# Performance work log

Measured on AMD Instinct MI355X. Metric: run time of the kernel, lower is better.

Reference implementation:

```python
import jax, jax.numpy as jnp
import numpy as np

B, S = 1024, 512
V, E, H, T = 50000, 300, 800, 50


def setup_inputs() -> dict:
    key = jax.random.key(0)
    ks = jax.random.split(key, 8)
    ids = jax.random.randint(ks[0], (B, S), 0, V, dtype=jnp.int64 if jax.config.jax_enable_x64 else jnp.int32)
    return {
        "ids": ids,
        "rho": jax.random.normal(ks[1], (V, E), jnp.float32) * 0.02,
        "alpha": jax.random.normal(ks[2], (T, E), jnp.float32) * 0.02,
        "W1": jax.random.normal(ks[3], (E, H), jnp.float32) * 0.05,
        "b1": jnp.zeros((H,), jnp.float32),
        "Wmu": jax.random.normal(ks[4], (H, T), jnp.float32) * 0.05,
        "bmu": jnp.zeros((T,), jnp.float32),
        "Wlv": jax.random.normal(ks[5], (H, T), jnp.float32) * 0.05,
        "blv": jnp.zeros((T,), jnp.float32),
    }


def reference(ids, rho, alpha, W1, b1, Wmu, bmu, Wlv, blv):
    b, s = ids.shape
    v = rho.shape[0]
    # bag-of-words histogram: scatter-add instead of dense one_hot+reduce_sum
    bows = jnp.zeros((b, v), rho.dtype).at[jnp.arange(b)[:, None], ids].add(1.0)
    # zero out special tokens 1 and 2 (original: x * (1 - sum(one_hot([1,2]))))
    bows = bows.at[:, jnp.array([1, 2])].set(0.0)
    normal_bows = bows / jnp.sum(bows, axis=-1, keepdims=True)
    # encoder (eval mode: dropout is identity)
    x = jnp.einsum('bv,ve->be', normal_bows, rho)
    h = jax.nn.relu(x @ W1 + b1)
    mu_theta = h @ Wmu + bmu
    logsigma_theta = h @ Wlv + blv
    kl_theta = -0.5 * jnp.sum(1.0 + logsigma_theta - mu_theta**2 - jnp.exp(logsigma_theta), axis=-1)
    # reparameterize (eval/inference mode): z = mu
    theta = jax.nn.softmax(mu_theta, axis=-1)  # [B, T]
    beta = jax.nn.softmax(jnp.einsum('te,ve->tv', alpha, rho), axis=-1)  # [T, V]
    lookup = jnp.log(theta @ beta + 1e-5)  # [B, V]
    recon_loss = -jnp.sum(lookup * bows, axis=-1)
    loss = jnp.mean(recon_loss) + jnp.mean(kl_theta)
    return theta, loss
```

## Files before the change

kernel.cpp:

```cpp
#include <hip/hip_runtime.h>
#include <math.h>


#define Bn 1024
#define Sn 512
#define Vn 50000
#define En 300
#define Hn 800
#define Tn 50
#define KP 320
#define BSTR 64
#define W1FRAG_N (50 * 10 * 64 * 8)
#define WFRAG_N  (8 * 25 * 64 * 8)
#define NRANGE 8
#define CASTB 7813
#define K4B 3128

typedef __bf16 bf16x8 __attribute__((ext_vector_type(8)));
typedef float  f32x4  __attribute__((ext_vector_type(4)));
typedef float  f32x2  __attribute__((ext_vector_type(2)));

__device__ __forceinline__ float waveReduceSum(float v) {
    #pragma unroll
    for (int off = 32; off > 0; off >>= 1) v += __shfl_xor(v, off, 64);
    return v;
}
__device__ __forceinline__ float waveReduceMax(float v) {
    #pragma unroll
    for (int off = 32; off > 0; off >>= 1) v = fmaxf(v, __shfl_xor(v, off, 64));
    return v;
}
__device__ __forceinline__ unsigned short f2bf(float x) {
    unsigned u = __float_as_uint(x);
    return (unsigned short)((u + 0x7FFFu + ((u >> 16) & 1u)) >> 16);
}
__device__ __forceinline__ float bf_lo(unsigned u) { return __uint_as_float(u << 16); }
__device__ __forceinline__ float bf_hi(unsigned u) { return __uint_as_float(u & 0xFFFF0000u); }
__device__ __forceinline__ int lane_prefix(unsigned long long m) {
    return __builtin_amdgcn_mbcnt_hi((unsigned)(m >> 32),
           __builtin_amdgcn_mbcnt_lo((unsigned)m, 0));
}

#define PKACC(u) { \
    c0 += (f32x2){bf_lo((u).x), bf_hi((u).x)}; \
    c1 += (f32x2){bf_lo((u).y), bf_hi((u).y)}; \
    c2 += (f32x2){bf_lo((u).z), bf_hi((u).z)}; \
    c3 += (f32x2){bf_lo((u).w), bf_hi((u).w)}; }

__global__ __launch_bounds__(256) void ka_init(
        const float4* __restrict__ rho4, unsigned short* __restrict__ rhoh,
        const float* __restrict__ alpha, const float* __restrict__ W1,
        const float* __restrict__ Wmu, const float* __restrict__ Wlv,
        unsigned short* __restrict__ bfrag, unsigned short* __restrict__ w1frag,
        unsigned short* __restrict__ wfrag, float* __restrict__ topicsumR,
        float* __restrict__ loss) {
    if (blockIdx.x < CASTB) {
        const int i = blockIdx.x * 256 + threadIdx.x;
        if (i < Vn * (KP / 8)) {
            int v = i / (KP / 8), s8 = i - v * (KP / 8);
            int c = s8 * 8;
            ushort4 o0 = {0, 0, 0, 0}, o1 = {0, 0, 0, 0};
            if (c < En) {
                float4 r = rho4[v * (En / 4) + s8 * 2];
                o0.x = f2bf(r.x); o0.y = f2bf(r.y); o0.z = f2bf(r.z); o0.w = f2bf(r.w);
            }
            if (c + 4 < En) {
                float4 r = rho4[v * (En / 4) + s8 * 2 + 1];
                o1.x = f2bf(r.x); o1.y = f2bf(r.y); o1.z = f2bf(r.z); o1.w = f2bf(r.w);
            }
            uint4 st;
            st.x = (unsigned)o0.x | ((unsigned)o0.y << 16);
            st.y = (unsigned)o0.z | ((unsigned)o0.w << 16);
            st.z = (unsigned)o1.x | ((unsigned)o1.y << 16);
            st.w = (unsigned)o1.z | ((unsigned)o1.w << 16);
            *(uint4*)(rhoh + (size_t)v * KP + c) = st;
        }
        return;
    }
    const int gid = (blockIdx.x - CASTB) * 256 + threadIdx.x;
    if (gid < 512) topicsumR[gid] = 0.f;
    if (gid == 520) *loss = 0.f;
    if (gid < 4 * 10 * 64 * 8) {
        int j = gid & 7;
        int lane = (gid >> 3) & 63;
        int rest = gid >> 9;
        int kt = rest % 10, w = rest / 10;
        int t = 16 * w + (lane & 15);
        int e = kt * 32 + (lane >> 4) * 8 + j;
        bfrag[gid] = (t < Tn && e < En) ? f2bf(alpha[t * En + e]) : (unsigned short)0;
    }
    if (gid < W1FRAG_N) {
        int j = gid & 7, lane = (gid >> 3) & 63, rest = gid >> 9;
        int kt = rest % 10, nt = rest / 10;
        int e = kt * 32 + (lane >> 4) * 8 + j;
        int hcol = nt * 16 + (lane & 15);
        w1frag[gid] = (e < En) ? f2bf(W1[e * Hn + hcol]) : (unsigned short)0;
    } else {
        int g2 = gid - W1FRAG_N;
        if (g2 < WFRAG_N) {
            int j = g2 & 7, lane = (g2 >> 3) & 63, rest = g2 >> 9;
            int kt = rest % 25, nt = rest / 25;
            int k = kt * 32 + (lane >> 4) * 8 + j;
            int t = (nt & 3) * 16 + (lane & 15);
            float val = 0.f;
            if (t < Tn) val = (nt < 4) ? Wmu[k * Tn + t] : Wlv[k * Tn + t];
            wfrag[g2] = f2bf(val);
        }
    }
}

__global__ __launch_bounds__(256) void kb_beta_tokens(
        const unsigned short* __restrict__ rhoh,
        const unsigned short* __restrict__ bfrag,
        unsigned int* __restrict__ betaU32, float* __restrict__ topicsumR,
        const int* __restrict__ ids, int* __restrict__ toks,
        int* __restrict__ cnt, float* __restrict__ xbarP) {
    __shared__ unsigned short trans[16 * 66];
    __shared__ __align__(16) int sid[Sn];
    __shared__ int sfid[Sn];
    __shared__ __align__(16) float xred[4][320];
    __shared__ int scount, sfull;
    const int tid = threadIdx.x;
    const int wave = tid >> 6, lane = tid & 63;

    if (blockIdx.x < K4B) {
        const int x = blockIdx.x & 7;
        const int n = blockIdx.x >> 3;
        const int tile = ((x * 3125) >> 3) + n;
        if (tile >= (((x + 1) * 3125) >> 3)) return;
        const int quad = lane >> 4, l15 = lane & 15;
        const int v0 = tile * 16;
        const unsigned short* arow = rhoh + (size_t)(v0 + l15) * KP + quad * 8;
        f32x4 acc = {0.f, 0.f, 0.f, 0.f};
        #pragma unroll
        for (int kt = 0; kt < 10; ++kt) {
            bf16x8 a = *(const bf16x8*)(arow + kt * 32);
            bf16x8 bv = *(const bf16x8*)(bfrag + ((wave * 10 + kt) * 64 + lane) * 8);
            acc = __builtin_amdgcn_mfma_f32_16x16x32_bf16(a, bv, acc, 0, 0, 0);
        }
        float ts = 0.f;
        #pragma unroll
        for (int r = 0; r < 4; ++r) {
            float ev = expf(acc[r]);
            ts += ev;
            trans[(quad * 4 + r) * 66 + 16 * wave + l15] = f2bf(ev);
        }
        ts += __shfl_xor(ts, 16, 64);
        ts += __shfl_xor(ts, 32, 64);
        const int t = 16 * wave + l15;
        if (lane < 16 && t < Tn)
            atomicAdd(&topicsumR[x * 64 + t], ts);
        __syncthreads();
        unsigned int* dst = betaU32 + (size_t)v0 * 32;
        const unsigned int* tr32 = (const unsigned int*)trans;
        for (int i = tid; i < 16 * 32; i += 256)
            __builtin_nontemporal_store(tr32[(i >> 5) * 33 + (i & 31)], &dst[i]);
        return;
    }
    const int blk = blockIdx.x - K4B;
    const int r = blk & (NRANGE - 1), b = blk >> 3;
    const int lo = ((r * 3125) >> 3) * 16;
    const int hi = (((r + 1) * 3125) >> 3) * 16;
    if (tid == 0) { scount = 0; sfull = 0; }
    __syncthreads();
    #pragma unroll
    for (int s0 = 0; s0 < Sn; s0 += 256) {
        int id = __builtin_nontemporal_load(&ids[b * Sn + s0 + tid]);
        bool val = (id != 1 && id != 2);
        bool inr = val && id >= lo && id < hi;
        unsigned long long mb = __ballot(inr);
        int pre = lane_prefix(mb);
        int wc = __popcll(mb);
        int base = 0;
        if (lane == 0 && wc) base = atomicAdd(&scount, wc);
        base = __shfl(base, 0, 64);
        if (inr) sid[base + pre] = id;
        if (r == 0) {
            unsigned long long fb = __ballot(val);
            int fpre = lane_prefix(fb);
            int fwc = __popcll(fb);
            int fbase = 0;
            if (lane == 0 && fwc) fbase = atomicAdd(&sfull, fwc);
            fbase = __shfl(fbase, 0, 64);
            if (val) sfid[fbase + fpre] = id;
        }
    }
    __syncthreads();
    if (r == 0) {
        const int nf = sfull;
        for (int i = tid; i < nf; i += 256)
            __builtin_nontemporal_store(sfid[i], &toks[b * Sn + i]);
        if (tid == 0) cnt[b] = nf;
    }
    const int m = scount;
    f32x2 c0 = {0.f, 0.f}, c1 = {0.f, 0.f}, c2 = {0.f, 0.f}, c3 = {0.f, 0.f};
    if (lane < 40) {
        const uint4* rb = (const uint4*)rhoh;
        int s = wave;
        for (; s + 12 < m; s += 16) {
            int i0 = sid[s], i1 = sid[s + 4], i2 = sid[s + 8], i3 = sid[s + 12];
            uint4 u0 = rb[(size_t)i0 * 40 + lane];
            uint4 u1 = rb[(size_t)i1 * 40 + lane];
            uint4 u2 = rb[(size_t)i2 * 40 + lane];
            uint4 u3 = rb[(size_t)i3 * 40 + lane];
            PKACC(u0); PKACC(u1); PKACC(u2); PKACC(u3);
        }
        for (; s < m; s += 4) {
            uint4 u = rb[(size_t)sid[s] * 40 + lane];
            PKACC(u);
        }
        float* xw = &xred[wave][lane * 8];
        *(float4*)(xw)     = (float4){c0[0], c0[1], c1[0], c1[1]};
        *(float4*)(xw + 4) = (float4){c2[0], c2[1], c3[0], c3[1]};
    }
    __syncthreads();
    float* xbp = xbarP + ((size_t)b * NRANGE + r) * KP;
    for (int c = tid; c < KP; c += 256)
        __builtin_nontemporal_store(
            xred[0][c] + xred[1][c] + xred[2][c] + xred[3][c], &xbp[c]);
}

__global__ __launch_bounds__(256) void ktail(
        const float* __restrict__ xbarP, const int* __restrict__ cnt,
        const unsigned short* __restrict__ w1frag, const float* __restrict__ b1,
        const unsigned short* __restrict__ wfrag,
        const float* __restrict__ bmu, const float* __restrict__ blv,
        float* __restrict__ theta, float* __restrict__ loss) {
    __shared__ unsigned short xs[16 * 328];
    __shared__ unsigned short hs[16 * 808];
    __shared__ float mlds[16 * 65];
    __shared__ float llds[16 * 65];
    __shared__ float invn[16];
    const int tid = threadIdx.x;
    const int wave = tid >> 6, lane = tid & 63;
    const int quad = lane >> 4, l15 = lane & 15;
    const int b0 = blockIdx.x * 16;
    if (tid < 16) invn[tid] = 1.0f / (float)cnt[b0 + tid];
    __syncthreads();
    for (int i = tid; i < 16 * (KP / 4); i += 256) {
        int row = i / (KP / 4), e4 = (i - row * (KP / 4)) * 4;
        const float* bp = xbarP + ((size_t)(b0 + row) * NRANGE) * KP + e4;
        float sx = 0.f, sy = 0.f, sz = 0.f, sw_ = 0.f;
        #pragma unroll
        for (int rr = 0; rr < NRANGE; ++rr) {
            float4 v = *(const float4*)(bp + rr * KP);
            sx += v.x; sy += v.y; sz += v.z; sw_ += v.w;
        }
        float in = invn[row];
        ushort4 o;
        o.x = f2bf(sx * in); o.y = f2bf(sy * in);
        o.z = f2bf(sz * in); o.w = f2bf(sw_ * in);
        *(ushort4*)&xs[row * 328 + e4] = o;
    }
    __syncthreads();
    {
        const unsigned short* arow = xs + l15 * 328 + quad * 8;
        for (int nt = wave; nt < 50; nt += 4) {
            f32x4 acc = {0.f, 0.f, 0.f, 0.f};
            #pragma unroll
            for (int kt = 0; kt < 10; ++kt) {
                bf16x8 a = *(const bf16x8*)(arow + kt * 32);
                bf16x8 bv = *(const bf16x8*)(w1frag + ((size_t)(nt * 10 + kt) * 64 + lane) * 8);
                acc = __builtin_amdgcn_mfma_f32_16x16x32_bf16(a, bv, acc, 0, 0, 0);
            }
            const int col = nt * 16 + l15;
            const float bias = b1[col];
            #pragma unroll
            for (int r = 0; r < 4; ++r)
                hs[(quad * 4 + r) * 808 + col] = f2bf(fmaxf(acc[r] + bias, 0.f));
        }
    }
    __syncthreads();
    {
        const unsigned short* arow = hs + l15 * 808 + quad * 8;
        f32x4 am = {0.f, 0.f, 0.f, 0.f}, al = {0.f, 0.f, 0.f, 0.f};
        #pragma unroll
        for (int kt = 0; kt < 25; ++kt) {
            bf16x8 a  = *(const bf16x8*)(arow + kt * 32);
            bf16x8 bm = *(const bf16x8*)(wfrag + ((size_t)(wave * 25 + kt) * 64 + lane) * 8);
            bf16x8 bl = *(const bf16x8*)(wfrag + ((size_t)((4 + wave) * 25 + kt) * 64 + lane) * 8);
            am = __builtin_amdgcn_mfma_f32_16x16x32_bf16(a, bm, am, 0, 0, 0);
            al = __builtin_amdgcn_mfma_f32_16x16x32_bf16(a, bl, al, 0, 0, 0);
        }
        const int t = wave * 16 + l15;
        const float bm_ = (t < Tn) ? bmu[t] : 0.f;
        const float bl_ = (t < Tn) ? blv[t] : 0.f;
        #pragma unroll
        for (int r = 0; r < 4; ++r) {
            int row = quad * 4 + r;
            mlds[row * 65 + t] = am[r] + bm_;
            llds[row * 65 + t] = al[r] + bl_;
        }
    }
    __syncthreads();
    const int tt = (lane < Tn) ? lane : (Tn - 1);
    const bool act = (lane < Tn);
    float klacc = 0.f;
    #pragma unroll
    for (int k = 0; k < 4; ++k) {
        int row = wave * 4 + k;
        float mu = mlds[row * 65 + tt];
        float lv = llds[row * 65 + tt];
        float m = waveReduceMax(act ? mu : -1e30f);
        float ex = act ? expf(mu - m) : 0.f;
        float ssum = waveReduceSum(ex);
        if (act) theta[(b0 + row) * Tn + lane] = ex / ssum;
        klacc += waveReduceSum(act ? (1.f + lv - mu * mu - expf(lv)) : 0.f);
    }
    if (lane == 0) atomicAdd(loss, -0.5f * klacc * (1.0f / (float)Bn));
}

__global__ __launch_bounds__(256) void k6_recon(
        const int* __restrict__ toks, const int* __restrict__ cnt,
        const float* __restrict__ theta, const float* __restrict__ topicsumR,
        const unsigned short* __restrict__ betaUh, float* __restrict__ loss) {
    __shared__ float sw[Tn];
    __shared__ float swred[4];
    const int b = blockIdx.x, tid = threadIdx.x;
    if (tid < Tn) {
        float z = 0.f;
        #pragma unroll
        for (int j = 0; j < 8; ++j) z += topicsumR[j * 64 + tid];
        sw[tid] = theta[b * Tn + tid] / z;
    }
    __syncthreads();
    float wr[Tn];
    #pragma unroll
    for (int t = 0; t < Tn; ++t) wr[t] = sw[t];
    float lsum = 0.f;
    const int n = cnt[b];
    for (int i = tid; i < n; i += 256) {
        int v = toks[b * Sn + i];
        const uint4* q = (const uint4*)(betaUh + (size_t)v * BSTR);
        float dot = 0.f;
        #pragma unroll
        for (int k = 0; k < 6; ++k) {
            uint4 u = q[k];
            int t = 8 * k;
            dot += wr[t]     * bf_lo(u.x) + wr[t + 1] * bf_hi(u.x);
            dot += wr[t + 2] * bf_lo(u.y) + wr[t + 3] * bf_hi(u.y);
            dot += wr[t + 4] * bf_lo(u.z) + wr[t + 5] * bf_hi(u.z);
            dot += wr[t + 6] * bf_lo(u.w) + wr[t + 7] * bf_hi(u.w);
        }
        unsigned d = ((const unsigned*)q)[24];
        dot += wr[48] * bf_lo(d) + wr[49] * bf_hi(d);
        lsum += logf(dot + 1e-5f);
    }
    float s = waveReduceSum(lsum);
    const int wave = tid >> 6, lane = tid & 63;
    if (lane == 0) swred[wave] = s;
    __syncthreads();
    if (tid == 0) {
        float tot = swred[0] + swred[1] + swred[2] + swred[3];
        atomicAdd(loss, -tot * (1.0f / (float)Bn));
    }
}

extern "C" void kernel_launch(void* const* d_in, const int* in_sizes, int n_in,
                              void* d_out, int out_size, void* d_ws, size_t ws_size,
                              hipStream_t stream) {
    const int*   ids   = (const int*)d_in[0];
    const float* rho   = (const float*)d_in[1];
    const float* alpha = (const float*)d_in[2];
    const float* W1    = (const float*)d_in[3];
    const float* b1    = (const float*)d_in[4];
    const float* Wmu   = (const float*)d_in[5];
    const float* bmu   = (const float*)d_in[6];
    const float* Wlv   = (const float*)d_in[7];
    const float* blv   = (const float*)d_in[8];

    float* theta = (float*)d_out;
    float* loss  = theta + Bn * Tn;

    char* w = (char*)d_ws;
    float* topicsumR = (float*)w;               w += 8 * 64 * 4;
    unsigned short* bfrag = (unsigned short*)w; w += 4 * 10 * 64 * 8 * 2;
    unsigned short* w1frag = (unsigned short*)w; w += (size_t)W1FRAG_N * 2;
    unsigned short* wfrag = (unsigned short*)w;  w += (size_t)WFRAG_N * 2;
    int*   cnt      = (int*)w;                  w += Bn * 4;
    int*   toks     = (int*)w;                  w += Bn * Sn * 4;
    float* xbarP    = (float*)w;                w += (size_t)Bn * NRANGE * KP * 4;
    unsigned short* rhoh = (unsigned short*)w;  w += (size_t)Vn * KP * 2;
    unsigned int* betaU32 = (unsigned int*)w;   w += (size_t)Vn * 128;

    const int k0grid = (W1FRAG_N + WFRAG_N + 255) / 256;
    ka_init<<<CASTB + k0grid, 256, 0, stream>>>(
        (const float4*)rho, rhoh, alpha, W1, Wmu, Wlv,
        bfrag, w1frag, wfrag, topicsumR, loss);
    kb_beta_tokens<<<K4B + Bn * NRANGE, 256, 0, stream>>>(
        rhoh, bfrag, betaU32, topicsumR, ids, toks, cnt, xbarP);
    ktail<<<64, 256, 0, stream>>>(xbarP, cnt, w1frag, b1, wfrag, bmu, blv,
                                  theta, loss);
    k6_recon<<<Bn, 256, 0, stream>>>(toks, cnt, theta, topicsumR,
                                     (const unsigned short*)betaU32, loss);
}
```

Before: 211.3 us.

## Fuse rho bf16 cast into beta kernel and split token gather kernel

The fp32-to-bf16 conversion of rho moves out of the init kernel and into the beta kernel. Each tile now loads fp32 rho rows, converts them into shared memory, writes the bf16 copy, and feeds the MFMA directly from LDS. The old combined beta/token kernel is split into two launches, kb4_beta and kb1_gather, and the nontemporal stores become plain stores. This avoids a full separate pass that reread rhoh before the beta GEMM, but it adds a kernel launch and serializes the beta and gather work that previously shared one grid.

```diff
diff --git a/kernel.cpp b/kernel.cpp
--- a/kernel.cpp
+++ b/kernel.cpp
@@ -13,7 +13,6 @@
 #define W1FRAG_N (50 * 10 * 64 * 8)
 #define WFRAG_N  (8 * 25 * 64 * 8)
 #define NRANGE 8
-#define CASTB 7813
 #define K4B 3128
 
 typedef __bf16 bf16x8 __attribute__((ext_vector_type(8)));
@@ -47,37 +46,13 @@
     c2 += (f32x2){bf_lo((u).z), bf_hi((u).z)}; \
     c3 += (f32x2){bf_lo((u).w), bf_hi((u).w)}; }
 
-__global__ __launch_bounds__(256) void ka_init(
-        const float4* __restrict__ rho4, unsigned short* __restrict__ rhoh,
+__global__ __launch_bounds__(256) void ka2_init(
         const float* __restrict__ alpha, const float* __restrict__ W1,
         const float* __restrict__ Wmu, const float* __restrict__ Wlv,
         unsigned short* __restrict__ bfrag, unsigned short* __restrict__ w1frag,
         unsigned short* __restrict__ wfrag, float* __restrict__ topicsumR,
         float* __restrict__ loss) {
-    if (blockIdx.x < CASTB) {
-        const int i = blockIdx.x * 256 + threadIdx.x;
-        if (i < Vn * (KP / 8)) {
-            int v = i / (KP / 8), s8 = i - v * (KP / 8);
-            int c = s8 * 8;
-            ushort4 o0 = {0, 0, 0, 0}, o1 = {0, 0, 0, 0};
-            if (c < En) {
-                float4 r = rho4[v * (En / 4) + s8 * 2];
-                o0.x = f2bf(r.x); o0.y = f2bf(r.y); o0.z = f2bf(r.z); o0.w = f2bf(r.w);
-            }
-            if (c + 4 < En) {
-                float4 r = rho4[v * (En / 4) + s8 * 2 + 1];
-                o1.x = f2bf(r.x); o1.y = f2bf(r.y); o1.z = f2bf(r.z); o1.w = f2bf(r.w);
-            }
-            uint4 st;
-            st.x = (unsigned)o0.x | ((unsigned)o0.y << 16);
-            st.y = (unsigned)o0.z | ((unsigned)o0.w << 16);
-            st.z = (unsigned)o1.x | ((unsigned)o1.y << 16);
-            st.w = (unsigned)o1.z | ((unsigned)o1.w << 16);
-            *(uint4*)(rhoh + (size_t)v * KP + c) = st;
-        }
-        return;
-    }
-    const int gid = (blockIdx.x - CASTB) * 256 + threadIdx.x;
+    const int gid = blockIdx.x * 256 + threadIdx.x;
     if (gid < 512) topicsumR[gid] = 0.f;
     if (gid == 520) *loss = 0.f;
     if (gid < 4 * 10 * 64 * 8) {
@@ -109,56 +84,72 @@
     }
 }
 
-__global__ __launch_bounds__(256) void kb_beta_tokens(
-        const unsigned short* __restrict__ rhoh,
+__global__ __launch_bounds__(256) void kb4_beta(
+        const float* __restrict__ rho, unsigned short* __restrict__ rhoh,
         const unsigned short* __restrict__ bfrag,
-        unsigned int* __restrict__ betaU32, float* __restrict__ topicsumR,
-        const int* __restrict__ ids, int* __restrict__ toks,
-        int* __restrict__ cnt, float* __restrict__ xbarP) {
+        unsigned int* __restrict__ betaU32, float* __restrict__ topicsumR) {
+    __shared__ __align__(16) unsigned short xs[16 * 328];
     __shared__ unsigned short trans[16 * 66];
+    const int x = blockIdx.x & 7;
+    const int n = blockIdx.x >> 3;
+    const int tile = ((x * 3125) >> 3) + n;
+    if (tile >= (((x + 1) * 3125) >> 3)) return;
+    const int tid = threadIdx.x;
+    const int wave = tid >> 6, lane = tid & 63;
+    const int quad = lane >> 4, l15 = lane & 15;
+    const int v0 = tile * 16;
+    for (int i = tid; i < 16 * 80; i += 256) {
+        int row = i / 80, s4 = i - row * 80;
+        ushort4 o = {0, 0, 0, 0};
+        if (s4 < 75) {
+            float4 r = *(const float4*)(rho + (size_t)(v0 + row) * En + s4 * 4);
+            o.x = f2bf(r.x); o.y = f2bf(r.y); o.z = f2bf(r.z); o.w = f2bf(r.w);
+        }
+        *(ushort4*)&xs[row * 328 + s4 * 4] = o;
+    }
+    __syncthreads();
+    for (int i = tid; i < 16 * 40; i += 256) {
+        int row = i / 40, c8 = (i - row * 40) * 8;
+        *(uint4*)(rhoh + (size_t)(v0 + row) * KP + c8) = *(const uint4*)&xs[row * 328 + c8];
+    }
+    const unsigned short* arow = xs + l15 * 328 + quad * 8;
+    f32x4 acc = {0.f, 0.f, 0.f, 0.f};
+    #pragma unroll
+    for (int kt = 0; kt < 10; ++kt) {
+        bf16x8 a = *(const bf16x8*)(arow + kt * 32);
+        bf16x8 bv = *(const bf16x8*)(bfrag + ((wave * 10 + kt) * 64 + lane) * 8);
+        acc = __builtin_amdgcn_mfma_f32_16x16x32_bf16(a, bv, acc, 0, 0, 0);
+    }
+    float ts = 0.f;
+    #pragma unroll
+    for (int r = 0; r < 4; ++r) {
+        float ev = expf(acc[r]);
+        ts += ev;
+        trans[(quad * 4 + r) * 66 + 16 * wave + l15] = f2bf(ev);
+    }
+    ts += __shfl_xor(ts, 16, 64);
+    ts += __shfl_xor(ts, 32, 64);
+    const int t = 16 * wave + l15;
+    if (lane < 16 && t < Tn)
+        atomicAdd(&topicsumR[x * 64 + t], ts);
+    __syncthreads();
+    unsigned int* dst = betaU32 + (size_t)v0 * 32;
+    const unsigned int* tr32 = (const unsigned int*)trans;
+    for (int i = tid; i < 16 * 32; i += 256)
+        dst[i] = tr32[(i >> 5) * 33 + (i & 31)];
+}
+
+__global__ __launch_bounds__(256) void kb1_gather(
+        const unsigned short* __restrict__ rhoh, const int* __restrict__ ids,
+        int* __restrict__ toks, int* __restrict__ cnt,
+        float* __restrict__ xbarP) {
     __shared__ __align__(16) int sid[Sn];
     __shared__ int sfid[Sn];
     __shared__ __align__(16) float xred[4][320];
     __shared__ int scount, sfull;
     const int tid = threadIdx.x;
     const int wave = tid >> 6, lane = tid & 63;
-
-    if (blockIdx.x < K4B) {
-        const int x = blockIdx.x & 7;
-        const int n = blockIdx.x >> 3;
-        const int tile = ((x * 3125) >> 3) + n;
-        if (tile >= (((x + 1) * 3125) >> 3)) return;
-        const int quad = lane >> 4, l15 = lane & 15;
-        const int v0 = tile * 16;
-        const unsigned short* arow = rhoh + (size_t)(v0 + l15) * KP + quad * 8;
-        f32x4 acc = {0.f, 0.f, 0.f, 0.f};
-        #pragma unroll
-        for (int kt = 0; kt < 10; ++kt) {
-            bf16x8 a = *(const bf16x8*)(arow + kt * 32);
-            bf16x8 bv = *(const bf16x8*)(bfrag + ((wave * 10 + kt) * 64 + lane) * 8);
-            acc = __builtin_amdgcn_mfma_f32_16x16x32_bf16(a, bv, acc, 0, 0, 0);
-        }
-        float ts = 0.f;
-        #pragma unroll
-        for (int r = 0; r < 4; ++r) {
-            float ev = expf(acc[r]);
-            ts += ev;
-            trans[(quad * 4 + r) * 66 + 16 * wave + l15] = f2bf(ev);
-        }
-        ts += __shfl_xor(ts, 16, 64);
-        ts += __shfl_xor(ts, 32, 64);
-        const int t = 16 * wave + l15;
-        if (lane < 16 && t < Tn)
-            atomicAdd(&topicsumR[x * 64 + t], ts);
-        __syncthreads();
-        unsigned int* dst = betaU32 + (size_t)v0 * 32;
-        const unsigned int* tr32 = (const unsigned int*)trans;
-        for (int i = tid; i < 16 * 32; i += 256)
-            __builtin_nontemporal_store(tr32[(i >> 5) * 33 + (i & 31)], &dst[i]);
-        return;
-    }
-    const int blk = blockIdx.x - K4B;
-    const int r = blk & (NRANGE - 1), b = blk >> 3;
+    const int r = blockIdx.x & (NRANGE - 1), b = blockIdx.x >> 3;
     const int lo = ((r * 3125) >> 3) * 16;
     const int hi = (((r + 1) * 3125) >> 3) * 16;
     if (tid == 0) { scount = 0; sfull = 0; }
@@ -188,8 +179,7 @@
     __syncthreads();
     if (r == 0) {
         const int nf = sfull;
-        for (int i = tid; i < nf; i += 256)
-            __builtin_nontemporal_store(sfid[i], &toks[b * Sn + i]);
+        for (int i = tid; i < nf; i += 256) toks[b * Sn + i] = sfid[i];
         if (tid == 0) cnt[b] = nf;
     }
     const int m = scount;
@@ -216,8 +206,7 @@
     __syncthreads();
     float* xbp = xbarP + ((size_t)b * NRANGE + r) * KP;
     for (int c = tid; c < KP; c += 256)
-        __builtin_nontemporal_store(
-            xred[0][c] + xred[1][c] + xred[2][c] + xred[3][c], &xbp[c]);
+        xbp[c] = xred[0][c] + xred[1][c] + xred[2][c] + xred[3][c];
 }
 
 __global__ __launch_bounds__(256) void ktail(
@@ -384,11 +373,10 @@
     unsigned int* betaU32 = (unsigned int*)w;   w += (size_t)Vn * 128;
 
     const int k0grid = (W1FRAG_N + WFRAG_N + 255) / 256;
-    ka_init<<<CASTB + k0grid, 256, 0, stream>>>(
-        (const float4*)rho, rhoh, alpha, W1, Wmu, Wlv,
-        bfrag, w1frag, wfrag, topicsumR, loss);
-    kb_beta_tokens<<<K4B + Bn * NRANGE, 256, 0, stream>>>(
-        rhoh, bfrag, betaU32, topicsumR, ids, toks, cnt, xbarP);
+    ka2_init<<<k0grid, 256, 0, stream>>>(
+        alpha, W1, Wmu, Wlv, bfrag, w1frag, wfrag, topicsumR, loss);
+    kb4_beta<<<K4B, 256, 0, stream>>>(rho, rhoh, bfrag, betaU32, topicsumR);
+    kb1_gather<<<Bn * NRANGE, 256, 0, stream>>>(rhoh, ids, toks, cnt, xbarP);
     ktail<<<64, 256, 0, stream>>>(xbarP, cnt, w1frag, b1, wfrag, bmu, blv,
                                   theta, loss);
     k6_recon<<<Bn, 256, 0, stream>>>(toks, cnt, theta, topicsumR,
```

Result: faster. 201.2 us, median of 2 (-4.8%).
